# Performance work log

Hardware: AMD Instinct MI355X
Metric: run time of the kernel (lower is better)

The kernel has to match this reference:

```python
import jax, jax.numpy as jnp
import numpy as np

N = 100000   # nodes
E = 1600000  # edges
F_IN = 32    # num_features
H = 16       # hidden_size (hardcoded as conv2 input in source)
C = 10       # num_classes
K = 2        # kernel_size (dim=1)


def setup_inputs() -> dict:
    key = jax.random.key(0)
    ks = jax.random.split(key, 9)
    x = jax.random.normal(ks[0], (N, F_IN), dtype=jnp.float32)
    edge_index = jax.random.randint(ks[1], (2, E), 0, N, dtype=jnp.int64)
    edge_attr = jax.random.uniform(ks[2], (E, 1), dtype=jnp.float32)
    s1 = 1.0 / np.sqrt(F_IN)
    s2 = 1.0 / np.sqrt(H)
    W1 = jax.random.normal(ks[3], (K, F_IN, H), dtype=jnp.float32) * s1
    root1 = jax.random.normal(ks[4], (F_IN, H), dtype=jnp.float32) * s1
    b1 = jnp.zeros((H,), dtype=jnp.float32)
    W2 = jax.random.normal(ks[5], (K, H, C), dtype=jnp.float32) * s2
    root2 = jax.random.normal(ks[6], (H, C), dtype=jnp.float32) * s2
    b2 = jnp.zeros((C,), dtype=jnp.float32)
    return {"x": x, "edge_index": edge_index, "edge_attr": edge_attr,
            "W1": W1, "root1": root1, "b1": b1,
            "W2": W2, "root2": root2, "b2": b2}


def spline_conv(x, edge_index, edge_attr, W, root, bias, num_nodes):
    # Open B-spline, degree 1: hat-function basis over K knots.
    k = W.shape[0]
    src, dst = edge_index[0], edge_index[1]
    v = edge_attr[:, 0] * (k - 1)                                   # [E]
    grid = jnp.arange(k, dtype=v.dtype)
    basis = jnp.maximum(0.0, 1.0 - jnp.abs(v[:, None] - grid[None, :]))  # [E,K]
    xe = x[src]                                                      # [E,in] gather
    msg = jnp.einsum('ei,kio,ek->eo', xe, W, basis)                  # per-edge message
    agg = jax.ops.segment_sum(msg, dst, num_segments=num_nodes)      # scatter-add
    deg = jax.ops.segment_sum(jnp.ones((msg.shape[0],), x.dtype), dst,
                              num_segments=num_nodes)
    agg = agg / jnp.maximum(deg, 1.0)[:, None]                       # mean aggregation
    return agg + x @ root + bias


def reference(x, edge_index, edge_attr, W1, root1, b1, W2, root2, b2):
    # Inference mode: F.dropout(training=False) is identity.
    h = jax.nn.elu(spline_conv(x, edge_index, edge_attr, W1, root1, b1, N))
    out = spline_conv(h, edge_index, edge_attr, W2, root2, b2, N)
    return jax.nn.log_softmax(out, axis=1)
```

## Files before the change

kernel.cpp:

```cpp
#include <hip/hip_runtime.h>
#include <math.h>

#define N_NODES 100000
#define E_EDGES 1600000
#define F_IN 32
#define HID 16
#define NC 10
#define SRC_BITS 17
#define SRC_MASK ((1u << SRC_BITS) - 1u)
#define VQ_SCALE 32767.0f
#define CBITS 10
#define BUCKET_N 1024
#define NCB 98
#define BLK_E 4096
#define NBLK ((E_EDGES + BLK_E - 1) / BLK_E)
#define NODE_GRID ((N_NODES + 255) / 256)

__device__ __forceinline__ unsigned int bf16pair(float lo, float hi) {
    unsigned int ulo = __float_as_uint(lo), uhi = __float_as_uint(hi);
    ulo += 0x7fffu + ((ulo >> 16) & 1u);
    uhi += 0x7fffu + ((uhi >> 16) & 1u);
    return (ulo >> 16) | (uhi & 0xffff0000u);
}

__device__ __forceinline__ float lerp_pair(unsigned int pair, float v) {
    float a = __uint_as_float(pair << 16);
    float b = __uint_as_float(pair & 0xffff0000u);
    return fmaf(v, b - a, a);
}

__global__ __launch_bounds__(256) void fused_l1cnt(
    const float* __restrict__ x, const float* __restrict__ W1,
    const float* __restrict__ root1, const float* __restrict__ b1,
    const int* __restrict__ ei,
    unsigned int* __restrict__ y, float* __restrict__ r1,
    int* __restrict__ cnt)
{
    if (blockIdx.x >= NODE_GRID) {
        __shared__ int h[NCB];
        int b = blockIdx.x - NODE_GRID;
        for (int i = threadIdx.x; i < NCB; i += 256) h[i] = 0;
        __syncthreads();
        int e0 = b * BLK_E;
        for (int i = threadIdx.x; i < BLK_E; i += 256) {
            int e = e0 + i;
            if (e < E_EDGES) atomicAdd(&h[ei[E_EDGES + e] >> CBITS], 1);
        }
        __syncthreads();
        for (int s = threadIdx.x; s < NCB; s += 256)
            cnt[s * NBLK + b] = h[s];
        return;
    }
    __shared__ float sW0[F_IN * HID], sW1[F_IN * HID], sR[F_IN * HID], sB[HID];
    for (int i = threadIdx.x; i < F_IN * HID; i += 256) {
        sW0[i] = W1[i];
        sW1[i] = W1[F_IN * HID + i];
        sR[i]  = root1[i];
    }
    if (threadIdx.x < HID) sB[threadIdx.x] = b1[threadIdx.x];
    __syncthreads();

    int n = blockIdx.x * 256 + threadIdx.x;
    if (n >= N_NODES) return;

    float xr[F_IN];
    const float4* xp = (const float4*)(x + (size_t)n * F_IN);
    #pragma unroll
    for (int i = 0; i < F_IN / 4; i++) {
        float4 t = xp[i];
        xr[i*4+0] = t.x; xr[i*4+1] = t.y; xr[i*4+2] = t.z; xr[i*4+3] = t.w;
    }

    float a0[HID], a1[HID], ar[HID];
    #pragma unroll
    for (int o = 0; o < HID; o++) { a0[o] = 0.f; a1[o] = 0.f; ar[o] = sB[o]; }
    for (int i = 0; i < F_IN; i++) {
        float xi = xr[i];
        #pragma unroll
        for (int o = 0; o < HID; o++) {
            a0[o] += xi * sW0[i * HID + o];
            a1[o] += xi * sW1[i * HID + o];
            ar[o] += xi * sR[i * HID + o];
        }
    }
    unsigned int* py = y + (size_t)n * 16;
    float* pr = r1 + (size_t)n * HID;
    #pragma unroll
    for (int o = 0; o < HID; o++) {
        py[o] = bf16pair(a0[o], a1[o]);
        pr[o] = ar[o];
    }
}

__global__ __launch_bounds__(512) void k_cscan(int* __restrict__ cnt,
                                               int* __restrict__ tsum)
{
    __shared__ int lds[512];
    int s = blockIdx.x, t = threadIdx.x;
    int v = (t < NBLK) ? cnt[s * NBLK + t] : 0;
    lds[t] = v;
    __syncthreads();
    #pragma unroll
    for (int off = 1; off < 512; off <<= 1) {
        int u = (t >= off) ? lds[t - off] : 0;
        __syncthreads();
        lds[t] += u;
        __syncthreads();
    }
    if (t < NBLK) cnt[s * NBLK + t] = lds[t] - v;
    if (t == 511) tsum[s] = lds[511];
}

__global__ __launch_bounds__(128) void k_tscan(const int* __restrict__ tsum,
                                               int* __restrict__ bucketBase,
                                               int* __restrict__ start)
{
    __shared__ int lds[128];
    int t = threadIdx.x;
    int v = (t < NCB) ? tsum[t] : 0;
    lds[t] = v;
    __syncthreads();
    #pragma unroll
    for (int off = 1; off < 128; off <<= 1) {
        int u = (t >= off) ? lds[t - off] : 0;
        __syncthreads();
        lds[t] += u;
        __syncthreads();
    }
    if (t < NCB) bucketBase[t] = lds[t] - v;
    if (t == 127) { bucketBase[NCB] = lds[127]; start[N_NODES] = lds[127]; }
}

__global__ __launch_bounds__(256) void k_bucket(
    const int* __restrict__ ei, const float* __restrict__ ea,
    const int* __restrict__ pref, const int* __restrict__ bucketBase,
    int2* __restrict__ ebuf)
{
    __shared__ int base[NCB], cur[NCB];
    for (int s = threadIdx.x; s < NCB; s += 256) {
        base[s] = bucketBase[s] + pref[s * NBLK + blockIdx.x];
        cur[s] = 0;
    }
    __syncthreads();
    int e0 = blockIdx.x * BLK_E;
    for (int i = threadIdx.x; i < BLK_E; i += 256) {
        int e = e0 + i;
        if (e >= E_EDGES) continue;
        int dst = ei[E_EDGES + e];
        int s = dst >> CBITS;
        int off = atomicAdd(&cur[s], 1);
        unsigned int vq = (unsigned int)(ea[e] * VQ_SCALE + 0.5f);
        unsigned int packed = (vq << SRC_BITS) | (unsigned int)ei[e];
        ebuf[base[s] + off] = make_int2(dst & (BUCKET_N - 1), (int)packed);
    }
}

__global__ __launch_bounds__(1024) void k_bsort(
    const int2* __restrict__ ebuf, const int* __restrict__ bucketBase,
    unsigned int* __restrict__ es, int* __restrict__ start)
{
    __shared__ int hist[BUCKET_N];
    __shared__ int cursor[BUCKET_N];
    __shared__ int wsum[16], woff[16];
    int t = threadIdx.x;
    int b = blockIdx.x;
    int j0 = bucketBase[b], j1 = bucketBase[b + 1];
    hist[t] = 0; cursor[t] = 0;
    __syncthreads();
    for (int j = j0 + t; j < j1; j += 1024)
        atomicAdd(&hist[ebuf[j].x], 1);
    __syncthreads();
    int c = hist[t];
    int w = t >> 6, l = t & 63;
    int incl = c;
    #pragma unroll
    for (int off = 1; off < 64; off <<= 1) {
        int u = __shfl_up(incl, off, 64);
        if (l >= off) incl += u;
    }
    if (l == 63) wsum[w] = incl;
    __syncthreads();
    if (t == 0) {
        int acc = 0;
        #pragma unroll
        for (int i = 0; i < 16; i++) { woff[i] = acc; acc += wsum[i]; }
    }
    __syncthreads();
    int excl = woff[w] + incl - c;
    hist[t] = excl;
    int node = (b << CBITS) + t;
    if (node < N_NODES) start[node] = j0 + excl;
    __syncthreads();
    for (int j = j0 + t; j < j1; j += 1024) {
        int2 p = ebuf[j];
        int off = atomicAdd(&cursor[p.x], 1);
        es[j0 + hist[p.x] + off] = (unsigned int)p.y;
    }
}

__global__ __launch_bounds__(256) void k_agg1(
    const unsigned int* __restrict__ es, const int* __restrict__ start,
    const unsigned int* __restrict__ y, const float* __restrict__ r1,
    const float* __restrict__ W2, const float* __restrict__ root2,
    const float* __restrict__ b2,
    unsigned int* __restrict__ z, float* __restrict__ r2)
{
    __shared__ float sh[16 * 17];
    __shared__ float sW0[HID * NC], sW1[HID * NC], sRt[HID * NC], sB2[NC];
    int t = threadIdx.x;
    if (t < HID * NC) { sW0[t] = W2[t]; sW1[t] = W2[HID * NC + t]; sRt[t] = root2[t]; }
    if (t >= HID * NC && t < HID * NC + NC) sB2[t - HID * NC] = b2[t - HID * NC];

    int idx = blockIdx.x * 256 + t;
    int n = idx >> 4, o = idx & 15, g = t >> 4;
    if (n < N_NODES) {
        int j0 = start[n], j1 = start[n + 1];
        float acc0 = 0.f, acc1 = 0.f, acc2 = 0.f, acc3 = 0.f;
        int j = j0;
        for (; j + 3 < j1; j += 4) {
            unsigned int p0 = es[j], p1 = es[j+1], p2 = es[j+2], p3 = es[j+3];
            unsigned int q0 = y[(size_t)(p0 & SRC_MASK) * 16 + o];
            unsigned int q1 = y[(size_t)(p1 & SRC_MASK) * 16 + o];
            unsigned int q2 = y[(size_t)(p2 & SRC_MASK) * 16 + o];
            unsigned int q3 = y[(size_t)(p3 & SRC_MASK) * 16 + o];
            acc0 += lerp_pair(q0, (float)(p0 >> SRC_BITS) * (1.0f / VQ_SCALE));
            acc1 += lerp_pair(q1, (float)(p1 >> SRC_BITS) * (1.0f / VQ_SCALE));
            acc2 += lerp_pair(q2, (float)(p2 >> SRC_BITS) * (1.0f / VQ_SCALE));
            acc3 += lerp_pair(q3, (float)(p3 >> SRC_BITS) * (1.0f / VQ_SCALE));
        }
        for (; j < j1; j++) {
            unsigned int p = es[j];
            unsigned int q = y[(size_t)(p & SRC_MASK) * 16 + o];
            acc0 += lerp_pair(q, (float)(p >> SRC_BITS) * (1.0f / VQ_SCALE));
        }
        float acc = (acc0 + acc1) + (acc2 + acc3);
        float inv = 1.0f / fmaxf((float)(j1 - j0), 1.0f);
        float hv = acc * inv + r1[(size_t)n * HID + o];
        sh[g * 17 + o] = hv > 0.0f ? hv : expm1f(hv);
    }
    __syncthreads();

    int n2 = blockIdx.x * 16 + g;
    if (n2 < N_NODES) {
        int cc = o;
        unsigned int* pz = z + (size_t)n2 * 16;
        if (cc < NC) {
            float a0 = 0.f, a1 = 0.f, ar = sB2[cc];
            #pragma unroll
            for (int i = 0; i < HID; i++) {
                float hi = sh[g * 17 + i];
                a0 += hi * sW0[i * NC + cc];
                a1 += hi * sW1[i * NC + cc];
                ar += hi * sRt[i * NC + cc];
            }
            pz[cc] = bf16pair(a0, a1);
            r2[(size_t)n2 * NC + cc] = ar;
        } else {
            pz[cc] = 0u;
        }
    }
}

__global__ __launch_bounds__(256) void k_agg2(
    const unsigned int* __restrict__ es, const int* __restrict__ start,
    const unsigned int* __restrict__ z,
    const float* __restrict__ r2, float* __restrict__ out)
{
    int idx = blockIdx.x * 256 + threadIdx.x;
    int n = idx >> 4, o = idx & 15;
    if (n >= N_NODES) return;
    int j0 = start[n], j1 = start[n + 1];
    float acc0 = 0.f, acc1 = 0.f, acc2 = 0.f, acc3 = 0.f;
    int j = j0;
    for (; j + 3 < j1; j += 4) {
        unsigned int p0 = es[j], p1 = es[j+1], p2 = es[j+2], p3 = es[j+3];
        unsigned int q0 = z[(size_t)(p0 & SRC_MASK) * 16 + o];
        unsigned int q1 = z[(size_t)(p1 & SRC_MASK) * 16 + o];
        unsigned int q2 = z[(size_t)(p2 & SRC_MASK) * 16 + o];
        unsigned int q3 = z[(size_t)(p3 & SRC_MASK) * 16 + o];
        acc0 += lerp_pair(q0, (float)(p0 >> SRC_BITS) * (1.0f / VQ_SCALE));
        acc1 += lerp_pair(q1, (float)(p1 >> SRC_BITS) * (1.0f / VQ_SCALE));
        acc2 += lerp_pair(q2, (float)(p2 >> SRC_BITS) * (1.0f / VQ_SCALE));
        acc3 += lerp_pair(q3, (float)(p3 >> SRC_BITS) * (1.0f / VQ_SCALE));
    }
    for (; j < j1; j++) {
        unsigned int p = es[j];
        unsigned int q = z[(size_t)(p & SRC_MASK) * 16 + o];
        acc0 += lerp_pair(q, (float)(p >> SRC_BITS) * (1.0f / VQ_SCALE));
    }
    float acc = (acc0 + acc1) + (acc2 + acc3);
    float val = -INFINITY;
    if (o < NC) {
        float inv = 1.0f / fmaxf((float)(j1 - j0), 1.0f);
        val = acc * inv + r2[(size_t)n * NC + o];
    }
    float mx = val;
    #pragma unroll
    for (int off = 8; off > 0; off >>= 1) mx = fmaxf(mx, __shfl_xor(mx, off, 16));
    float ex = (o < NC) ? expf(val - mx) : 0.0f;
    float ssum = ex;
    #pragma unroll
    for (int off = 8; off > 0; off >>= 1) ssum += __shfl_xor(ssum, off, 16);
    if (o < NC) out[(size_t)n * NC + o] = val - mx - logf(ssum);
}

extern "C" void kernel_launch(void* const* d_in, const int* in_sizes, int n_in,
                              void* d_out, int out_size, void* d_ws, size_t ws_size,
                              hipStream_t stream) {
    const float* x     = (const float*)d_in[0];
    const int*   ei    = (const int*)d_in[1];
    const float* ea    = (const float*)d_in[2];
    const float* W1    = (const float*)d_in[3];
    const float* root1 = (const float*)d_in[4];
    const float* b1    = (const float*)d_in[5];
    const float* W2    = (const float*)d_in[6];
    const float* root2 = (const float*)d_in[7];
    const float* b2    = (const float*)d_in[8];
    float* out = (float*)d_out;

    char* wsb = (char*)d_ws;
    int2*         ebuf   = (int2*)wsb;
    unsigned int* es     = (unsigned int*)(wsb + (size_t)E_EDGES * 8);
    unsigned int* y      = es + (size_t)E_EDGES;
    float*        r1     = (float*)(y + (size_t)N_NODES * 16);
    unsigned int* z      = (unsigned int*)(r1 + (size_t)N_NODES * HID);
    float*        r2     = (float*)(z + (size_t)N_NODES * 16);
    int*          start  = (int*)(r2 + (size_t)N_NODES * NC);
    int*          cnt    = start + N_NODES + 1;
    int*          tsum   = cnt + NCB * NBLK;
    int*          bucketBase = tsum + NCB;

    int aggGrid  = (N_NODES * 16 + 255) / 256;

    fused_l1cnt<<<NODE_GRID + NBLK, 256, 0, stream>>>(x, W1, root1, b1, ei, y, r1, cnt);
    k_cscan <<<NCB, 512, 0, stream>>>(cnt, tsum);
    k_tscan <<<1, 128, 0, stream>>>(tsum, bucketBase, start);
    k_bucket<<<NBLK, 256, 0, stream>>>(ei, ea, cnt, bucketBase, ebuf);
    k_bsort <<<NCB, 1024, 0, stream>>>(ebuf, bucketBase, es, start);
    k_agg1  <<<aggGrid, 256, 0, stream>>>(es, start, y, r1, W2, root2, b2, z, r2);
    k_agg2  <<<aggGrid, 256, 0, stream>>>(es, start, z, r2, out);
}
```

Baseline: 199.8 us.

## Halve bucket size, drop bucket-total scan kernel, unroll gathers by eight

Buckets shrink from 1024 to 512 nodes, which gives 196 coarse buckets and twice as many sort blocks, each with 512 threads. The separate single-block kernel that scanned bucket totals is removed. Every k_bucket and k_bsort block now redoes that small scan in shared memory, and start[N] is written directly from the edge count. The aggregation loops gain an 8-way unrolled main loop so more independent gathers are in flight per thread. The changes trade one launch and a serial dependency for redundant per-block scans and more registers in the aggregation kernels.

```diff
diff --git a/kernel.cpp b/kernel.cpp
--- a/kernel.cpp
+++ b/kernel.cpp
@@ -9,9 +9,9 @@
 #define SRC_BITS 17
 #define SRC_MASK ((1u << SRC_BITS) - 1u)
 #define VQ_SCALE 32767.0f
-#define CBITS 10
-#define BUCKET_N 1024
-#define NCB 98
+#define CBITS 9
+#define BUCKET_N 512
+#define NCB ((N_NODES + BUCKET_N - 1) / BUCKET_N)
 #define BLK_E 4096
 #define NBLK ((E_EDGES + BLK_E - 1) / BLK_E)
 #define NODE_GRID ((N_NODES + 255) / 256)
@@ -93,7 +93,8 @@
 }
 
 __global__ __launch_bounds__(512) void k_cscan(int* __restrict__ cnt,
-                                               int* __restrict__ tsum)
+                                               int* __restrict__ tsum,
+                                               int* __restrict__ start)
 {
     __shared__ int lds[512];
     int s = blockIdx.x, t = threadIdx.x;
@@ -109,41 +110,34 @@
     }
     if (t < NBLK) cnt[s * NBLK + t] = lds[t] - v;
     if (t == 511) tsum[s] = lds[511];
-}
-
-__global__ __launch_bounds__(128) void k_tscan(const int* __restrict__ tsum,
-                                               int* __restrict__ bucketBase,
-                                               int* __restrict__ start)
-{
-    __shared__ int lds[128];
+    if (s == 0 && t == 0) start[N_NODES] = E_EDGES;
+}
+
+__global__ __launch_bounds__(256) void k_bucket(
+    const int* __restrict__ ei, const float* __restrict__ ea,
+    const int* __restrict__ pref, const int* __restrict__ tsum,
+    int2* __restrict__ ebuf)
+{
+    __shared__ int sbb[256];
+    __shared__ int base[NCB], cur[NCB];
     int t = threadIdx.x;
     int v = (t < NCB) ? tsum[t] : 0;
-    lds[t] = v;
-    __syncthreads();
-    #pragma unroll
-    for (int off = 1; off < 128; off <<= 1) {
-        int u = (t >= off) ? lds[t - off] : 0;
-        __syncthreads();
-        lds[t] += u;
-        __syncthreads();
-    }
-    if (t < NCB) bucketBase[t] = lds[t] - v;
-    if (t == 127) { bucketBase[NCB] = lds[127]; start[N_NODES] = lds[127]; }
-}
-
-__global__ __launch_bounds__(256) void k_bucket(
-    const int* __restrict__ ei, const float* __restrict__ ea,
-    const int* __restrict__ pref, const int* __restrict__ bucketBase,
-    int2* __restrict__ ebuf)
-{
-    __shared__ int base[NCB], cur[NCB];
-    for (int s = threadIdx.x; s < NCB; s += 256) {
-        base[s] = bucketBase[s] + pref[s * NBLK + blockIdx.x];
-        cur[s] = 0;
+    sbb[t] = v;
+    __syncthreads();
+    #pragma unroll
+    for (int off = 1; off < 256; off <<= 1) {
+        int u = (t >= off) ? sbb[t - off] : 0;
+        __syncthreads();
+        sbb[t] += u;
+        __syncthreads();
+    }
+    if (t < NCB) {
+        base[t] = (sbb[t] - v) + pref[t * NBLK + blockIdx.x];
+        cur[t] = 0;
     }
     __syncthreads();
     int e0 = blockIdx.x * BLK_E;
-    for (int i = threadIdx.x; i < BLK_E; i += 256) {
+    for (int i = t; i < BLK_E; i += 256) {
         int e = e0 + i;
         if (e >= E_EDGES) continue;
         int dst = ei[E_EDGES + e];
@@ -155,19 +149,33 @@
     }
 }
 
-__global__ __launch_bounds__(1024) void k_bsort(
-    const int2* __restrict__ ebuf, const int* __restrict__ bucketBase,
+__global__ __launch_bounds__(512) void k_bsort(
+    const int2* __restrict__ ebuf, const int* __restrict__ tsum,
     unsigned int* __restrict__ es, int* __restrict__ start)
 {
+    __shared__ int sbb[256];
     __shared__ int hist[BUCKET_N];
     __shared__ int cursor[BUCKET_N];
-    __shared__ int wsum[16], woff[16];
+    __shared__ int wsum[8], woff[8];
     int t = threadIdx.x;
     int b = blockIdx.x;
-    int j0 = bucketBase[b], j1 = bucketBase[b + 1];
+    int v = 0;
+    if (t < 256) { v = (t < NCB) ? tsum[t] : 0; sbb[t] = v; }
+    __syncthreads();
+    #pragma unroll
+    for (int off = 1; off < 256; off <<= 1) {
+        int u = 0;
+        if (t < 256 && t >= off) u = sbb[t - off];
+        __syncthreads();
+        if (t < 256) sbb[t] += u;
+        __syncthreads();
+    }
+    int m  = tsum[b];
+    int j0 = sbb[b] - m;
+    int j1 = j0 + m;
     hist[t] = 0; cursor[t] = 0;
     __syncthreads();
-    for (int j = j0 + t; j < j1; j += 1024)
+    for (int j = j0 + t; j < j1; j += 512)
         atomicAdd(&hist[ebuf[j].x], 1);
     __syncthreads();
     int c = hist[t];
@@ -183,7 +191,7 @@
     if (t == 0) {
         int acc = 0;
         #pragma unroll
-        for (int i = 0; i < 16; i++) { woff[i] = acc; acc += wsum[i]; }
+        for (int i = 0; i < 8; i++) { woff[i] = acc; acc += wsum[i]; }
     }
     __syncthreads();
     int excl = woff[w] + incl - c;
@@ -191,7 +199,7 @@
     int node = (b << CBITS) + t;
     if (node < N_NODES) start[node] = j0 + excl;
     __syncthreads();
-    for (int j = j0 + t; j < j1; j += 1024) {
+    for (int j = j0 + t; j < j1; j += 512) {
         int2 p = ebuf[j];
         int off = atomicAdd(&cursor[p.x], 1);
         es[j0 + hist[p.x] + off] = (unsigned int)p.y;
@@ -217,6 +225,26 @@
         int j0 = start[n], j1 = start[n + 1];
         float acc0 = 0.f, acc1 = 0.f, acc2 = 0.f, acc3 = 0.f;
         int j = j0;
+        for (; j + 7 < j1; j += 8) {
+            unsigned int p0 = es[j],   p1 = es[j+1], p2 = es[j+2], p3 = es[j+3];
+            unsigned int p4 = es[j+4], p5 = es[j+5], p6 = es[j+6], p7 = es[j+7];
+            unsigned int q0 = y[(size_t)(p0 & SRC_MASK) * 16 + o];
+            unsigned int q1 = y[(size_t)(p1 & SRC_MASK) * 16 + o];
+            unsigned int q2 = y[(size_t)(p2 & SRC_MASK) * 16 + o];
+            unsigned int q3 = y[(size_t)(p3 & SRC_MASK) * 16 + o];
+            unsigned int q4 = y[(size_t)(p4 & SRC_MASK) * 16 + o];
+            unsigned int q5 = y[(size_t)(p5 & SRC_MASK) * 16 + o];
+            unsigned int q6 = y[(size_t)(p6 & SRC_MASK) * 16 + o];
+            unsigned int q7 = y[(size_t)(p7 & SRC_MASK) * 16 + o];
+            acc0 += lerp_pair(q0, (float)(p0 >> SRC_BITS) * (1.0f / VQ_SCALE));
+            acc1 += lerp_pair(q1, (float)(p1 >> SRC_BITS) * (1.0f / VQ_SCALE));
+            acc2 += lerp_pair(q2, (float)(p2 >> SRC_BITS) * (1.0f / VQ_SCALE));
+            acc3 += lerp_pair(q3, (float)(p3 >> SRC_BITS) * (1.0f / VQ_SCALE));
+            acc0 += lerp_pair(q4, (float)(p4 >> SRC_BITS) * (1.0f / VQ_SCALE));
+            acc1 += lerp_pair(q5, (float)(p5 >> SRC_BITS) * (1.0f / VQ_SCALE));
+            acc2 += lerp_pair(q6, (float)(p6 >> SRC_BITS) * (1.0f / VQ_SCALE));
+            acc3 += lerp_pair(q7, (float)(p7 >> SRC_BITS) * (1.0f / VQ_SCALE));
+        }
         for (; j + 3 < j1; j += 4) {
             unsigned int p0 = es[j], p1 = es[j+1], p2 = es[j+2], p3 = es[j+3];
             unsigned int q0 = y[(size_t)(p0 & SRC_MASK) * 16 + o];
@@ -272,6 +300,26 @@
     int j0 = start[n], j1 = start[n + 1];
     float acc0 = 0.f, acc1 = 0.f, acc2 = 0.f, acc3 = 0.f;
     int j = j0;
+    for (; j + 7 < j1; j += 8) {
+        unsigned int p0 = es[j],   p1 = es[j+1], p2 = es[j+2], p3 = es[j+3];
+        unsigned int p4 = es[j+4], p5 = es[j+5], p6 = es[j+6], p7 = es[j+7];
+        unsigned int q0 = z[(size_t)(p0 & SRC_MASK) * 16 + o];
+        unsigned int q1 = z[(size_t)(p1 & SRC_MASK) * 16 + o];
+        unsigned int q2 = z[(size_t)(p2 & SRC_MASK) * 16 + o];
+        unsigned int q3 = z[(size_t)(p3 & SRC_MASK) * 16 + o];
+        unsigned int q4 = z[(size_t)(p4 & SRC_MASK) * 16 + o];
+        unsigned int q5 = z[(size_t)(p5 & SRC_MASK) * 16 + o];
+        unsigned int q6 = z[(size_t)(p6 & SRC_MASK) * 16 + o];
+        unsigned int q7 = z[(size_t)(p7 & SRC_MASK) * 16 + o];
+        acc0 += lerp_pair(q0, (float)(p0 >> SRC_BITS) * (1.0f / VQ_SCALE));
+        acc1 += lerp_pair(q1, (float)(p1 >> SRC_BITS) * (1.0f / VQ_SCALE));
+        acc2 += lerp_pair(q2, (float)(p2 >> SRC_BITS) * (1.0f / VQ_SCALE));
+        acc3 += lerp_pair(q3, (float)(p3 >> SRC_BITS) * (1.0f / VQ_SCALE));
+        acc0 += lerp_pair(q4, (float)(p4 >> SRC_BITS) * (1.0f / VQ_SCALE));
+        acc1 += lerp_pair(q5, (float)(p5 >> SRC_BITS) * (1.0f / VQ_SCALE));
+        acc2 += lerp_pair(q6, (float)(p6 >> SRC_BITS) * (1.0f / VQ_SCALE));
+        acc3 += lerp_pair(q7, (float)(p7 >> SRC_BITS) * (1.0f / VQ_SCALE));
+    }
     for (; j + 3 < j1; j += 4) {
         unsigned int p0 = es[j], p1 = es[j+1], p2 = es[j+2], p3 = es[j+3];
         unsigned int q0 = z[(size_t)(p0 & SRC_MASK) * 16 + o];
@@ -328,15 +376,13 @@
     int*          start  = (int*)(r2 + (size_t)N_NODES * NC);
     int*          cnt    = start + N_NODES + 1;
     int*          tsum   = cnt + NCB * NBLK;
-    int*          bucketBase = tsum + NCB;
 
     int aggGrid  = (N_NODES * 16 + 255) / 256;
 
     fused_l1cnt<<<NODE_GRID + NBLK, 256, 0, stream>>>(x, W1, root1, b1, ei, y, r1, cnt);
-    k_cscan <<<NCB, 512, 0, stream>>>(cnt, tsum);
-    k_tscan <<<1, 128, 0, stream>>>(tsum, bucketBase, start);
-    k_bucket<<<NBLK, 256, 0, stream>>>(ei, ea, cnt, bucketBase, ebuf);
-    k_bsort <<<NCB, 1024, 0, stream>>>(ebuf, bucketBase, es, start);
+    k_cscan <<<NCB, 512, 0, stream>>>(cnt, tsum, start);
+    k_bucket<<<NBLK, 256, 0, stream>>>(ei, ea, cnt, tsum, ebuf);
+    k_bsort <<<NCB, 512, 0, stream>>>(ebuf, tsum, es, start);
     k_agg1  <<<aggGrid, 256, 0, stream>>>(es, start, y, r1, W2, root2, b2, z, r2);
     k_agg2  <<<aggGrid, 256, 0, stream>>>(es, start, z, r2, out);
 }
```

After: 191.8 us. 1.04x faster.
